# Optimization experiments

Measured on AMD Instinct MI355X. Metric: run time of the kernel, lower is better.

Reference implementation:

```python
import jax, jax.numpy as jnp
import numpy as np

BS, N = 64, 44            # batch, nodes per graph (fully connected)
H = 256                   # hidden_nf
N_LAYERS = 4              # equivariant blocks
INV_SUB = 2               # GCL sublayers per block
IN_H = 7                  # h feature dim incl. time channel (in_node_nf)
REP_NF = 512
NORM_FACTOR = 100.0       # normalization_factor, aggregation='sum'


def setup_inputs() -> dict:
    key = jax.random.key(0)
    ks = jax.random.split(key, 24)
    f32 = jnp.float32
    def rn(k, shape, s=0.02):
        return jax.random.normal(k, shape, f32) * s
    G = N_LAYERS * INV_SUB
    inp = {}
    inp['t'] = jax.random.uniform(ks[0], (BS, 1), f32)
    inp['xh'] = jax.random.normal(ks[1], (BS, N, 9), f32)
    inp['node_mask'] = jnp.ones((BS, N, 1), f32)
    # fully-connected edge mask with self-edges removed (standard EDM setup)
    inp['edge_mask'] = jnp.ones((BS, N, N, 1), f32) * (1.0 - jnp.eye(N, dtype=f32))[None, :, :, None]
    inp['rep'] = jax.random.normal(ks[2], (BS, REP_NF), f32)
    # parameters
    inp['W_embed'] = rn(ks[3], (IN_H, H)); inp['b_embed'] = jnp.zeros((H,), f32)
    inp['W_rep'] = rn(ks[4], (REP_NF, H)); inp['b_rep'] = jnp.zeros((H,), f32)
    # GCL stacks (edge_attr has 2 features: current + initial squared distance)
    inp['We1'] = rn(ks[5], (G, 2 * H + 2, H)); inp['be1'] = jnp.zeros((G, H), f32)
    inp['We2'] = rn(ks[6], (G, H, H));         inp['be2'] = jnp.zeros((G, H), f32)
    inp['Wn1'] = rn(ks[7], (G, 2 * H, H));     inp['bn1'] = jnp.zeros((G, H), f32)
    inp['Wn2'] = rn(ks[8], (G, H, H));         inp['bn2'] = jnp.zeros((G, H), f32)
    # coordinate-update MLP stacks (last layer bias-free, small init)
    inp['Wc1'] = rn(ks[9], (N_LAYERS, 2 * H + 2, H)); inp['bc1'] = jnp.zeros((N_LAYERS, H), f32)
    inp['Wc2'] = rn(ks[10], (N_LAYERS, H, H));        inp['bc2'] = jnp.zeros((N_LAYERS, H), f32)
    inp['Wc3'] = rn(ks[11], (N_LAYERS, H, 1), s=0.001)
    inp['W_out'] = rn(ks[12], (H, IN_H)); inp['b_out'] = jnp.zeros((IN_H,), f32)
    return inp


def _coord2diff(x):
    diff = x[:, :, None, :] - x[:, None, :, :]           # [bs,n,n,3]
    radial = jnp.sum(diff * diff, -1, keepdims=True)     # [bs,n,n,1] squared distance
    coord_diff = diff / jnp.sqrt(radial + 1e-8)          # norm_constant = 0
    return radial, coord_diff


def reference(t, xh, node_mask, edge_mask, rep,
              W_embed, b_embed, W_rep, b_rep,
              We1, be1, We2, be2, Wn1, bn1, Wn2, bn2,
              Wc1, bc1, Wc2, bc2, Wc3, W_out, b_out):
    silu = jax.nn.silu
    bs, n, _ = xh.shape
    xh = xh * node_mask
    x0 = xh[..., :3]
    h = xh[..., 3:]
    # condition_time: append per-graph time broadcast to nodes
    h = jnp.concatenate([h, jnp.broadcast_to(t[:, None, :], (bs, n, 1))], -1)
    # node embedding + per-graph rep conditioning (GeoRCG)
    h = h @ W_embed + b_embed + (rep @ W_rep + b_rep)[:, None, :]

    d0, _ = _coord2diff(x0)   # initial squared distances, reused as edge_attr base
    x = x0
    k = 0
    for l in range(N_LAYERS):
        d, cdiff = _coord2diff(x)
        ea = jnp.concatenate([d, d0], -1)                 # [bs,n,n,2]
        for _s in range(INV_SUB):
            hi = jnp.broadcast_to(h[:, :, None, :], (bs, n, n, H))
            hj = jnp.broadcast_to(h[:, None, :, :], (bs, n, n, H))
            e_in = jnp.concatenate([hi, hj, ea], -1)      # [bs,n,n,2H+2]
            m = silu(silu(e_in @ We1[k] + be1[k]) @ We2[k] + be2[k])
            m = m * edge_mask
            agg = jnp.sum(m, axis=2) / NORM_FACTOR        # scatter-sum over senders j
            h = h + (silu(jnp.concatenate([h, agg], -1) @ Wn1[k] + bn1[k]) @ Wn2[k] + bn2[k])
            h = h * node_mask
            k += 1
        # equivariant coordinate update
        hi = jnp.broadcast_to(h[:, :, None, :], (bs, n, n, H))
        hj = jnp.broadcast_to(h[:, None, :, :], (bs, n, n, H))
        e_in = jnp.concatenate([hi, hj, ea], -1)
        phi = silu(silu(e_in @ Wc1[l] + bc1[l]) @ Wc2[l] + bc2[l]) @ Wc3[l]  # [bs,n,n,1]
        trans = cdiff * phi * edge_mask
        x = (x + jnp.sum(trans, axis=2) / NORM_FACTOR) * node_mask

    h = (h @ W_out + b_out) * node_mask
    h_final = h[..., :-1]                                 # strip time channel
    vel = (x - x0) * node_mask
    # remove_mean_with_mask
    Nn = jnp.sum(node_mask, axis=1, keepdims=True)
    vel = (vel - jnp.sum(vel, axis=1, keepdims=True) / Nn) * node_mask
    return jnp.concatenate([vel, h_final], -1)            # [bs,n,9]
```

## Files before the change

kernel.cpp:

```cpp
#include <hip/hip_runtime.h>

typedef __bf16 bf16_t;
typedef __bf16 bf16x8 __attribute__((ext_vector_type(8)));
typedef float  f32x4  __attribute__((ext_vector_type(4)));

#define BSZ 64
#define NNODE 44
#define NODES (BSZ*NNODE)

__device__ __forceinline__ float  bf2f(bf16_t v){ return (float)v; }
__device__ __forceinline__ bf16_t f2bf(float v){ return (bf16_t)v; }
__device__ __forceinline__ float  silu_f(float v){ return v / (1.0f + __expf(-v)); }

__global__ void transpose_wb(const float* __restrict__ src, bf16_t* __restrict__ dst,
                             int R, int ldo) {
  __shared__ bf16_t tile[32][33];
  int g = blockIdx.z;
  src += (size_t)g * R * 256;
  dst += (size_t)g * 256 * ldo;
  int n0 = blockIdx.x * 32, r0 = blockIdx.y * 32;
  int tx = threadIdx.x, ty = threadIdx.y;
  for (int p = 0; p < 32; p += 8) {
    int r = r0 + ty + p;
    if (r < R) tile[ty + p][tx] = f2bf(src[(size_t)r * 256 + n0 + tx]);
  }
  __syncthreads();
  for (int p = 0; p < 32; p += 8) {
    int r = r0 + tx;
    if (r < R) dst[(size_t)(n0 + ty + p) * ldo + r] = tile[tx][ty + p];
  }
}

__global__ __launch_bounds__(256)
void repproj_kernel(const float* __restrict__ rep, const float* __restrict__ W_rep,
                    const float* __restrict__ b_rep, float* __restrict__ out) {
  int b = blockIdx.x, c = threadIdx.x;
  float acc = b_rep[c];
  const float* r = rep + (size_t)b * 512;
  for (int k = 0; k < 512; k++) acc += r[k] * W_rep[(size_t)k * 256 + c];
  out[(size_t)b * 256 + c] = acc;
}

__global__ __launch_bounds__(256)
void embed_kernel(const float* __restrict__ xh, const float* __restrict__ t,
                  const float* __restrict__ nmask,
                  const float* __restrict__ W_embed, const float* __restrict__ b_embed,
                  const float* __restrict__ repproj,
                  float* __restrict__ h_f32, bf16_t* __restrict__ cat1,
                  float* __restrict__ x0, float* __restrict__ x) {
  int m = blockIdx.x;
  int b = m / NNODE;
  int c = threadIdx.x;
  float nm = nmask[m];
  float acc = b_embed[c] + repproj[(size_t)b * 256 + c];
  for (int kk = 0; kk < 6; kk++)
    acc += xh[(size_t)m * 9 + 3 + kk] * nm * W_embed[(size_t)kk * 256 + c];
  acc += t[b] * W_embed[6 * 256 + c];
  h_f32[(size_t)m * 256 + c] = acc;
  cat1 [(size_t)m * 512 + c] = f2bf(acc);
  if (c < 3) {
    float xv = xh[(size_t)m * 9 + c] * nm;
    x0[(size_t)m * 3 + c] = xv;
    x [(size_t)m * 3 + c] = xv;
  }
}

template<int MODE>
__global__ __launch_bounds__(256)
void gemm_node(const bf16_t* __restrict__ A, int lda,
               const bf16_t* __restrict__ BT, int ldbt,
               const float* __restrict__ bias, size_t ob, int K,
               float* __restrict__ outPQ,
               bf16_t* __restrict__ outB,
               const float* __restrict__ hold,
               float* __restrict__ hnew,
               bf16_t* __restrict__ catb,
               const float* __restrict__ nmask) {
  int tid = threadIdx.x;
  int m0 = blockIdx.y * 64, n0 = blockIdx.x * 64;
  int kof = (MODE == 0) ? (int)blockIdx.z * 256 : 0;
  int w = tid >> 6, lane = tid & 63, q = lane >> 4, lr = lane & 15;
  int wm = w & 1, wn = w >> 1;
  f32x4 acc[2][2];
  for (int a = 0; a < 2; a++) for (int bb = 0; bb < 2; bb++)
    for (int rr = 0; rr < 4; rr++) acc[a][bb][rr] = 0.0f;
  const bf16_t* Arow0 = A  + (size_t)(m0 + wm * 32 + lr) * lda;
  const bf16_t* Brow0 = BT + (size_t)(n0 + wn * 32 + lr) * ldbt + kof;
  for (int k0 = 0; k0 < K; k0 += 32) {
    bf16x8 af[2], bfr[2];
    for (int mt = 0; mt < 2; mt++)
      af[mt]  = *(const bf16x8*)(Arow0 + (size_t)mt * 16 * lda + k0 + q * 8);
    for (int nt = 0; nt < 2; nt++)
      bfr[nt] = *(const bf16x8*)(Brow0 + (size_t)nt * 16 * ldbt + k0 + q * 8);
    for (int mt = 0; mt < 2; mt++)
      for (int nt = 0; nt < 2; nt++)
        acc[mt][nt] = __builtin_amdgcn_mfma_f32_16x16x32_bf16(af[mt], bfr[nt], acc[mt][nt], 0, 0, 0);
  }
  for (int mt = 0; mt < 2; mt++)
    for (int nt = 0; nt < 2; nt++) {
      int col = n0 + wn * 32 + nt * 16 + lr;
      for (int rr = 0; rr < 4; rr++) {
        int row = m0 + wm * 32 + mt * 16 + q * 4 + rr;
        float v = acc[mt][nt][rr];
        if constexpr (MODE == 0) {
          outPQ[(size_t)row * 512 + (size_t)blockIdx.z * 256 + col] = v;
        } else if constexpr (MODE == 1) {
          v = silu_f(v + bias[ob + col]);
          outB[(size_t)row * 256 + col] = f2bf(v);
        } else {
          v = v + bias[ob + col] + hold[(size_t)row * 256 + col];
          v *= nmask[row];
          hnew[(size_t)row * 256 + col] = v;
          catb[(size_t)row * 512 + col] = f2bf(v);
        }
      }
    }
}

template<int COORD>
__global__ __launch_bounds__(256)
void edge_kernel(const float* __restrict__ PQ,
                 const float* __restrict__ We1raw, size_t oW1,
                 const float* __restrict__ be1,   size_t ob1,
                 const bf16_t* __restrict__ W2T,  size_t oW2,
                 const float* __restrict__ b2,    size_t ob2,
                 const float* __restrict__ wc3,   size_t oc3,
                 const float* __restrict__ xcur,
                 const float* __restrict__ x0g,
                 const float* __restrict__ emask,
                 const float* __restrict__ nmask,
                 bf16_t* __restrict__ aggout,
                 float* __restrict__ xnext) {
  __shared__ __align__(16) bf16_t Ae[48][264];
  __shared__ float  xjL[48][3], x0jL[48][3];
  __shared__ float2 ddL[48];
  __shared__ float  emLDS[48];
  __shared__ float  phiLDS[4][48];
  int ni = blockIdx.x;
  int b = ni / NNODE;
  int i = ni % NNODE;
  size_t e0 = (size_t)ni * NNODE;
  int tid = threadIdx.x;
  if (tid < NNODE) {
    for (int c = 0; c < 3; c++) {
      xjL [tid][c] = xcur[(size_t)(b * NNODE + tid) * 3 + c];
      x0jL[tid][c] = x0g [(size_t)(b * NNODE + tid) * 3 + c];
    }
  }
  if (tid < 48) emLDS[tid] = (tid < NNODE) ? emask[e0 + tid] : 0.f;
  __syncthreads();
  if (tid < NNODE) {
    float dx = xjL[i][0] - xjL[tid][0];
    float dy = xjL[i][1] - xjL[tid][1];
    float dz = xjL[i][2] - xjL[tid][2];
    float dd = dx * dx + dy * dy + dz * dz;
    float ex = x0jL[i][0] - x0jL[tid][0];
    float ey = x0jL[i][1] - x0jL[tid][1];
    float ez = x0jL[i][2] - x0jL[tid][2];
    float dd0 = ex * ex + ey * ey + ez * ez;
    ddL[tid] = make_float2(dd, dd0);
  }
  __syncthreads();
  {
    int n = tid;
    float pi_b = PQ[(size_t)ni * 512 + n] + be1[ob1 + n];
    float w512 = We1raw[oW1 + 512 * 256 + n];
    float w513 = We1raw[oW1 + 513 * 256 + n];
    const float* qptr = PQ + (size_t)(b * NNODE) * 512 + 256 + n;
    #pragma unroll 4
    for (int j = 0; j < NNODE; j++) {
      float2 dd = ddL[j];
      float v = silu_f(pi_b + qptr[(size_t)j * 512] + dd.x * w512 + dd.y * w513);
      Ae[j][n] = f2bf(v);
    }
    for (int j = NNODE; j < 48; j++) Ae[j][n] = (bf16_t)0.f;
  }
  __syncthreads();
  int w = tid >> 6, lane = tid & 63, q = lane >> 4, lr = lane & 15;
  f32x4 acc[3][4];
  for (int mt = 0; mt < 3; mt++) for (int nt = 0; nt < 4; nt++)
    for (int rr = 0; rr < 4; rr++) acc[mt][nt][rr] = 0.0f;
  const bf16_t* Bbase = W2T + oW2 + (size_t)(w * 64 + lr) * 256;
  #pragma unroll
  for (int kk = 0; kk < 256; kk += 32) {
    bf16x8 af[3], bfr[4];
    for (int mt = 0; mt < 3; mt++)
      af[mt]  = *(const bf16x8*)(&Ae[mt * 16 + lr][kk + q * 8]);
    for (int nt = 0; nt < 4; nt++)
      bfr[nt] = *(const bf16x8*)(Bbase + (size_t)nt * 16 * 256 + kk + q * 8);
    for (int mt = 0; mt < 3; mt++)
      for (int nt = 0; nt < 4; nt++)
        acc[mt][nt] = __builtin_amdgcn_mfma_f32_16x16x32_bf16(af[mt], bfr[nt], acc[mt][nt], 0, 0, 0);
  }
  if constexpr (!COORD) {
    for (int nt = 0; nt < 4; nt++) {
      int col = w * 64 + nt * 16 + lr;
      float bcol = b2[ob2 + col];
      float s = 0.f;
      for (int mt = 0; mt < 3; mt++)
        for (int rr = 0; rr < 4; rr++) {
          int row = mt * 16 + q * 4 + rr;
          s += silu_f(acc[mt][nt][rr] + bcol) * emLDS[row];
        }
      s += __shfl_xor(s, 16, 64);
      s += __shfl_xor(s, 32, 64);
      if (q == 0) aggout[(size_t)ni * 512 + 256 + col] = f2bf(s * 0.01f);
    }
  } else {
    for (int mt = 0; mt < 3; mt++) {
      float rs[4] = {0.f, 0.f, 0.f, 0.f};
      for (int nt = 0; nt < 4; nt++) {
        int col = w * 64 + nt * 16 + lr;
        float bcol = b2[ob2 + col];
        float wc   = wc3[oc3 + col];
        for (int rr = 0; rr < 4; rr++)
          rs[rr] += silu_f(acc[mt][nt][rr] + bcol) * wc;
      }
      for (int off = 1; off <= 8; off <<= 1)
        for (int rr = 0; rr < 4; rr++) rs[rr] += __shfl_xor(rs[rr], off, 64);
      if (lr == 0)
        for (int rr = 0; rr < 4; rr++)
          phiLDS[w][mt * 16 + q * 4 + rr] = rs[rr];
    }
    __syncthreads();
    if (tid < 64) {
      int j = lane;
      float tx = 0.f, ty = 0.f, tz = 0.f;
      if (j < NNODE) {
        float ph = 0.f;
        for (int ww = 0; ww < 4; ww++) ph += phiLDS[ww][j];
        ph *= emLDS[j];
        float dx = xjL[i][0] - xjL[j][0];
        float dy = xjL[i][1] - xjL[j][1];
        float dz = xjL[i][2] - xjL[j][2];
        float dd = dx * dx + dy * dy + dz * dz;
        float rinv = 1.0f / sqrtf(dd + 1e-8f);
        tx = ph * dx * rinv;
        ty = ph * dy * rinv;
        tz = ph * dz * rinv;
      }
      for (int off = 1; off <= 32; off <<= 1) {
        tx += __shfl_xor(tx, off, 64);
        ty += __shfl_xor(ty, off, 64);
        tz += __shfl_xor(tz, off, 64);
      }
      if (lane == 0) {
        float nm = nmask[ni];
        xnext[(size_t)ni * 3 + 0] = (xjL[i][0] + tx * 0.01f) * nm;
        xnext[(size_t)ni * 3 + 1] = (xjL[i][1] + ty * 0.01f) * nm;
        xnext[(size_t)ni * 3 + 2] = (xjL[i][2] + tz * 0.01f) * nm;
      }
    }
  }
}

__global__ __launch_bounds__(256)
void out_kernel(const float* __restrict__ h, const float* __restrict__ x,
                const float* __restrict__ x0, const float* __restrict__ nmask,
                const float* __restrict__ W_out, const float* __restrict__ b_out,
                float* __restrict__ out) {
  __shared__ float vel[NNODE][3];
  __shared__ float sums[4];
  int b = blockIdx.x, tid = threadIdx.x;
  if (tid < NNODE * 3) {
    int n = tid / 3, c = tid % 3;
    int m = b * NNODE + n;
    vel[n][c] = (x[(size_t)m * 3 + c] - x0[(size_t)m * 3 + c]) * nmask[m];
  }
  __syncthreads();
  if (tid < 4) {
    float s = 0.f;
    if (tid < 3) { for (int n = 0; n < NNODE; n++) s += vel[n][tid]; }
    else         { for (int n = 0; n < NNODE; n++) s += nmask[b * NNODE + n]; }
    sums[tid] = s;
  }
  __syncthreads();
  if (tid < NNODE * 3) {
    int n = tid / 3, c = tid % 3;
    int m = b * NNODE + n;
    float v = (vel[n][c] - sums[c] / sums[3]) * nmask[m];
    out[(size_t)m * 9 + c] = v;
  }
  for (int idx = tid; idx < NNODE * 6; idx += 256) {
    int n = idx / 6, c = idx % 6;
    int m = b * NNODE + n;
    float accv = b_out[c];
    const float* hr = h + (size_t)m * 256;
    for (int k = 0; k < 256; k++) accv += hr[k] * W_out[(size_t)k * 7 + c];
    out[(size_t)m * 9 + 3 + c] = accv * nmask[m];
  }
}

extern "C" void kernel_launch(void* const* d_in, const int* in_sizes, int n_in,
                              void* d_out, int out_size, void* d_ws, size_t ws_size,
                              hipStream_t stream) {
  const float* t       = (const float*)d_in[0];
  const float* xh      = (const float*)d_in[1];
  const float* nmask   = (const float*)d_in[2];
  const float* emask   = (const float*)d_in[3];
  const float* rep     = (const float*)d_in[4];
  const float* W_embed = (const float*)d_in[5];
  const float* b_embed = (const float*)d_in[6];
  const float* W_rep   = (const float*)d_in[7];
  const float* b_rep   = (const float*)d_in[8];
  const float* We1     = (const float*)d_in[9];
  const float* be1     = (const float*)d_in[10];
  const float* We2     = (const float*)d_in[11];
  const float* be2     = (const float*)d_in[12];
  const float* Wn1     = (const float*)d_in[13];
  const float* bn1     = (const float*)d_in[14];
  const float* Wn2     = (const float*)d_in[15];
  const float* bn2     = (const float*)d_in[16];
  const float* Wc1     = (const float*)d_in[17];
  const float* bc1     = (const float*)d_in[18];
  const float* Wc2     = (const float*)d_in[19];
  const float* bc2     = (const float*)d_in[20];
  const float* Wc3     = (const float*)d_in[21];
  const float* W_out   = (const float*)d_in[22];
  const float* b_out   = (const float*)d_in[23];

  char* p = (char*)d_ws;
  auto alloc = [&](size_t bytes) { char* r = p; p += (bytes + 255) & ~(size_t)255; return r; };
  bf16_t* We1T  = (bf16_t*)alloc((size_t)8 * 256 * 520 * 2);
  bf16_t* Wc1T  = (bf16_t*)alloc((size_t)4 * 256 * 520 * 2);
  bf16_t* We2T  = (bf16_t*)alloc((size_t)8 * 256 * 256 * 2);
  bf16_t* Wc2T  = (bf16_t*)alloc((size_t)4 * 256 * 256 * 2);
  bf16_t* Wn1T  = (bf16_t*)alloc((size_t)8 * 256 * 512 * 2);
  bf16_t* Wn2T  = (bf16_t*)alloc((size_t)8 * 256 * 256 * 2);
  float*  h_f32 = (float*) alloc((size_t)NODES * 256 * 4);
  bf16_t* cat1  = (bf16_t*)alloc((size_t)NODES * 512 * 2);
  bf16_t* t1    = (bf16_t*)alloc((size_t)NODES * 256 * 2);
  float*  PQ    = (float*) alloc((size_t)NODES * 512 * 4);
  float*  x0buf = (float*) alloc((size_t)NODES * 3 * 4);
  float*  xA    = (float*) alloc((size_t)NODES * 3 * 4);
  float*  xB    = (float*) alloc((size_t)NODES * 3 * 4);
  float*  rproj = (float*) alloc((size_t)BSZ * 256 * 4);

  dim3 tb(32, 8);
  transpose_wb<<<dim3(8, 17, 8), tb, 0, stream>>>(We1, We1T, 514, 520);
  transpose_wb<<<dim3(8, 17, 4), tb, 0, stream>>>(Wc1, Wc1T, 514, 520);
  transpose_wb<<<dim3(8,  8, 8), tb, 0, stream>>>(We2, We2T, 256, 256);
  transpose_wb<<<dim3(8,  8, 4), tb, 0, stream>>>(Wc2, Wc2T, 256, 256);
  transpose_wb<<<dim3(8, 16, 8), tb, 0, stream>>>(Wn1, Wn1T, 512, 512);
  transpose_wb<<<dim3(8,  8, 8), tb, 0, stream>>>(Wn2, Wn2T, 256, 256);

  repproj_kernel<<<BSZ, 256, 0, stream>>>(rep, W_rep, b_rep, rproj);
  embed_kernel<<<NODES, 256, 0, stream>>>(xh, t, nmask, W_embed, b_embed, rproj,
                                          h_f32, cat1, x0buf, xA);

  float* xcur = xA;
  for (int l = 0; l < 4; l++) {
    float* xnext = (l & 1) ? xA : xB;
    for (int s = 0; s < 2; s++) {
      int k = 2 * l + s;
      size_t oWe1 = (size_t)k * 514 * 256, obe1 = (size_t)k * 256;
      size_t oWe2 = (size_t)k * 256 * 256, obe2 = (size_t)k * 256;
      size_t obn1 = (size_t)k * 256, obn2 = (size_t)k * 256;
      gemm_node<0><<<dim3(4, 44, 2), 256, 0, stream>>>(
          cat1, 512, We1T + (size_t)k * 256 * 520, 520, nullptr, 0, 256,
          PQ, nullptr, nullptr, nullptr, nullptr, nullptr);
      edge_kernel<0><<<NODES, 256, 0, stream>>>(
          PQ, We1, oWe1, be1, obe1, We2T, oWe2, be2, obe2, Wc3, 0,
          xcur, x0buf, emask, nmask, cat1, nullptr);
      gemm_node<1><<<dim3(4, 44, 1), 256, 0, stream>>>(
          cat1, 512, Wn1T + (size_t)k * 256 * 512, 512, bn1, obn1, 512,
          nullptr, t1, nullptr, nullptr, nullptr, nullptr);
      gemm_node<2><<<dim3(4, 44, 1), 256, 0, stream>>>(
          t1, 256, Wn2T + (size_t)k * 256 * 256, 256, bn2, obn2, 256,
          nullptr, nullptr, h_f32, h_f32, cat1, nmask);
    }
    size_t oWc1 = (size_t)l * 514 * 256, obc1 = (size_t)l * 256;
    size_t oWc2 = (size_t)l * 256 * 256, obc2 = (size_t)l * 256;
    size_t oc3  = (size_t)l * 256;
    gemm_node<0><<<dim3(4, 44, 2), 256, 0, stream>>>(
        cat1, 512, Wc1T + (size_t)l * 256 * 520, 520, nullptr, 0, 256,
        PQ, nullptr, nullptr, nullptr, nullptr, nullptr);
    edge_kernel<1><<<NODES, 256, 0, stream>>>(
        PQ, Wc1, oWc1, bc1, obc1, Wc2T, oWc2, bc2, obc2, Wc3, oc3,
        xcur, x0buf, emask, nmask, nullptr, xnext);
    xcur = xnext;
  }

  out_kernel<<<BSZ, 256, 0, stream>>>(h_f32, xcur, x0buf, nmask, W_out, b_out,
                                      (float*)d_out);
}
```

Baseline: 1.233 ms.

## Fuse node MLP GEMMs and process two receiver nodes per edge block

New measurement: 1.239 ms. About the same (+0.5%).

```diff
diff --git a/kernel.cpp b/kernel.cpp
--- a/kernel.cpp
+++ b/kernel.cpp
@@ -65,20 +65,13 @@
   }
 }
 
-template<int MODE>
 __global__ __launch_bounds__(256)
-void gemm_node(const bf16_t* __restrict__ A, int lda,
-               const bf16_t* __restrict__ BT, int ldbt,
-               const float* __restrict__ bias, size_t ob, int K,
-               float* __restrict__ outPQ,
-               bf16_t* __restrict__ outB,
-               const float* __restrict__ hold,
-               float* __restrict__ hnew,
-               bf16_t* __restrict__ catb,
-               const float* __restrict__ nmask) {
+void gemm_pq(const bf16_t* __restrict__ A, int lda,
+             const bf16_t* __restrict__ BT, int ldbt,
+             float* __restrict__ outPQ) {
   int tid = threadIdx.x;
   int m0 = blockIdx.y * 64, n0 = blockIdx.x * 64;
-  int kof = (MODE == 0) ? (int)blockIdx.z * 256 : 0;
+  int kof = (int)blockIdx.z * 256;
   int w = tid >> 6, lane = tid & 63, q = lane >> 4, lr = lane & 15;
   int wm = w & 1, wn = w >> 1;
   f32x4 acc[2][2];
@@ -86,7 +79,7 @@
     for (int rr = 0; rr < 4; rr++) acc[a][bb][rr] = 0.0f;
   const bf16_t* Arow0 = A  + (size_t)(m0 + wm * 32 + lr) * lda;
   const bf16_t* Brow0 = BT + (size_t)(n0 + wn * 32 + lr) * ldbt + kof;
-  for (int k0 = 0; k0 < K; k0 += 32) {
+  for (int k0 = 0; k0 < 256; k0 += 32) {
     bf16x8 af[2], bfr[2];
     for (int mt = 0; mt < 2; mt++)
       af[mt]  = *(const bf16x8*)(Arow0 + (size_t)mt * 16 * lda + k0 + q * 8);
@@ -101,27 +94,81 @@
       int col = n0 + wn * 32 + nt * 16 + lr;
       for (int rr = 0; rr < 4; rr++) {
         int row = m0 + wm * 32 + mt * 16 + q * 4 + rr;
-        float v = acc[mt][nt][rr];
-        if constexpr (MODE == 0) {
-          outPQ[(size_t)row * 512 + (size_t)blockIdx.z * 256 + col] = v;
-        } else if constexpr (MODE == 1) {
-          v = silu_f(v + bias[ob + col]);
-          outB[(size_t)row * 256 + col] = f2bf(v);
-        } else {
-          v = v + bias[ob + col] + hold[(size_t)row * 256 + col];
-          v *= nmask[row];
-          hnew[(size_t)row * 256 + col] = v;
-          catb[(size_t)row * 512 + col] = f2bf(v);
-        }
+        outPQ[(size_t)row * 512 + (size_t)blockIdx.z * 256 + col] = acc[mt][nt][rr];
+      }
+    }
+}
+
+__global__ __launch_bounds__(256)
+void node_mlp(const bf16_t* __restrict__ cat1,
+              const bf16_t* __restrict__ Wn1T,
+              const float* __restrict__ bn1, size_t ob1,
+              const bf16_t* __restrict__ Wn2T,
+              const float* __restrict__ bn2, size_t ob2,
+              const float* __restrict__ nmask,
+              float* __restrict__ h, bf16_t* __restrict__ catb) {
+  __shared__ __align__(16) bf16_t t1s[64][264];
+  int tid = threadIdx.x;
+  int m0 = blockIdx.x * 64;
+  int w = tid >> 6, lane = tid & 63, q = lane >> 4, lr = lane & 15;
+  f32x4 acc[4][4];
+  for (int mt = 0; mt < 4; mt++) for (int nt = 0; nt < 4; nt++)
+    for (int rr = 0; rr < 4; rr++) acc[mt][nt][rr] = 0.0f;
+  const bf16_t* Arow = cat1 + (size_t)(m0 + lr) * 512;
+  const bf16_t* Brow = Wn1T + (size_t)(w * 64 + lr) * 512;
+  for (int k0 = 0; k0 < 512; k0 += 32) {
+    bf16x8 af[4], bfr[4];
+    for (int mt = 0; mt < 4; mt++)
+      af[mt]  = *(const bf16x8*)(Arow + (size_t)mt * 16 * 512 + k0 + q * 8);
+    for (int nt = 0; nt < 4; nt++)
+      bfr[nt] = *(const bf16x8*)(Brow + (size_t)nt * 16 * 512 + k0 + q * 8);
+    for (int mt = 0; mt < 4; mt++)
+      for (int nt = 0; nt < 4; nt++)
+        acc[mt][nt] = __builtin_amdgcn_mfma_f32_16x16x32_bf16(af[mt], bfr[nt], acc[mt][nt], 0, 0, 0);
+  }
+  for (int mt = 0; mt < 4; mt++)
+    for (int nt = 0; nt < 4; nt++) {
+      int col = w * 64 + nt * 16 + lr;
+      float bc = bn1[ob1 + col];
+      for (int rr = 0; rr < 4; rr++) {
+        int row = mt * 16 + q * 4 + rr;
+        t1s[row][col] = f2bf(silu_f(acc[mt][nt][rr] + bc));
+      }
+    }
+  __syncthreads();
+  f32x4 acc2[4][4];
+  for (int mt = 0; mt < 4; mt++) for (int nt = 0; nt < 4; nt++)
+    for (int rr = 0; rr < 4; rr++) acc2[mt][nt][rr] = 0.0f;
+  const bf16_t* Brow2 = Wn2T + (size_t)(w * 64 + lr) * 256;
+  for (int k0 = 0; k0 < 256; k0 += 32) {
+    bf16x8 af[4], bfr[4];
+    for (int mt = 0; mt < 4; mt++)
+      af[mt]  = *(const bf16x8*)(&t1s[mt * 16 + lr][k0 + q * 8]);
+    for (int nt = 0; nt < 4; nt++)
+      bfr[nt] = *(const bf16x8*)(Brow2 + (size_t)nt * 16 * 256 + k0 + q * 8);
+    for (int mt = 0; mt < 4; mt++)
+      for (int nt = 0; nt < 4; nt++)
+        acc2[mt][nt] = __builtin_amdgcn_mfma_f32_16x16x32_bf16(af[mt], bfr[nt], acc2[mt][nt], 0, 0, 0);
+  }
+  for (int mt = 0; mt < 4; mt++)
+    for (int nt = 0; nt < 4; nt++) {
+      int col = w * 64 + nt * 16 + lr;
+      float bc = bn2[ob2 + col];
+      for (int rr = 0; rr < 4; rr++) {
+        int row = m0 + mt * 16 + q * 4 + rr;
+        float v = acc2[mt][nt][rr] + bc + h[(size_t)row * 256 + col];
+        v *= nmask[row];
+        h[(size_t)row * 256 + col] = v;
+        catb[(size_t)row * 512 + col] = f2bf(v);
       }
     }
 }
 
 template<int COORD>
-__global__ __launch_bounds__(256)
+__global__ __launch_bounds__(512, 4)
 void edge_kernel(const float* __restrict__ PQ,
+                 const float* __restrict__ be1,   size_t ob1,
                  const float* __restrict__ We1raw, size_t oW1,
-                 const float* __restrict__ be1,   size_t ob1,
                  const bf16_t* __restrict__ W2T,  size_t oW2,
                  const float* __restrict__ b2,    size_t ob2,
                  const float* __restrict__ wc3,   size_t oc3,
@@ -131,15 +178,14 @@
                  const float* __restrict__ nmask,
                  bf16_t* __restrict__ aggout,
                  float* __restrict__ xnext) {
-  __shared__ __align__(16) bf16_t Ae[48][264];
+  __shared__ __align__(16) bf16_t Ae[96][264];
   __shared__ float  xjL[48][3], x0jL[48][3];
-  __shared__ float2 ddL[48];
-  __shared__ float  emLDS[48];
-  __shared__ float  phiLDS[4][48];
-  int ni = blockIdx.x;
-  int b = ni / NNODE;
-  int i = ni % NNODE;
-  size_t e0 = (size_t)ni * NNODE;
+  __shared__ float2 ddL[2][48];
+  __shared__ float  emLDS[2][48];
+  __shared__ float  phiLDS[8][96];
+  int bp = blockIdx.x;
+  int b  = bp / 22;
+  int ip = (bp % 22) * 2;
   int tid = threadIdx.x;
   if (tid < NNODE) {
     for (int c = 0; c < 3; c++) {
@@ -147,70 +193,85 @@
       x0jL[tid][c] = x0g [(size_t)(b * NNODE + tid) * 3 + c];
     }
   }
-  if (tid < 48) emLDS[tid] = (tid < NNODE) ? emask[e0 + tid] : 0.f;
-  __syncthreads();
-  if (tid < NNODE) {
-    float dx = xjL[i][0] - xjL[tid][0];
-    float dy = xjL[i][1] - xjL[tid][1];
-    float dz = xjL[i][2] - xjL[tid][2];
-    float dd = dx * dx + dy * dy + dz * dz;
-    float ex = x0jL[i][0] - x0jL[tid][0];
-    float ey = x0jL[i][1] - x0jL[tid][1];
-    float ez = x0jL[i][2] - x0jL[tid][2];
-    float dd0 = ex * ex + ey * ey + ez * ez;
-    ddL[tid] = make_float2(dd, dd0);
+  if (tid < 96) {
+    int ii = tid / 48, j = tid % 48;
+    emLDS[ii][j] = (j < NNODE) ? emask[(size_t)(b * NNODE + ip + ii) * NNODE + j] : 0.f;
+  }
+  __syncthreads();
+  if (tid < 96) {
+    int ii = tid / 48, j = tid % 48;
+    int i = ip + ii;
+    float2 r = make_float2(0.f, 0.f);
+    if (j < NNODE) {
+      float dx = xjL[i][0] - xjL[j][0];
+      float dy = xjL[i][1] - xjL[j][1];
+      float dz = xjL[i][2] - xjL[j][2];
+      r.x = dx * dx + dy * dy + dz * dz;
+      float ex = x0jL[i][0] - x0jL[j][0];
+      float ey = x0jL[i][1] - x0jL[j][1];
+      float ez = x0jL[i][2] - x0jL[j][2];
+      r.y = ex * ex + ey * ey + ez * ez;
+    }
+    ddL[ii][j] = r;
   }
   __syncthreads();
   {
-    int n = tid;
+    int n = tid & 255, half = tid >> 8;
+    int ni = b * NNODE + ip + half;
     float pi_b = PQ[(size_t)ni * 512 + n] + be1[ob1 + n];
     float w512 = We1raw[oW1 + 512 * 256 + n];
     float w513 = We1raw[oW1 + 513 * 256 + n];
     const float* qptr = PQ + (size_t)(b * NNODE) * 512 + 256 + n;
-    #pragma unroll 4
+    bf16_t* arow = &Ae[half * 48][0];
+    #pragma unroll 8
     for (int j = 0; j < NNODE; j++) {
-      float2 dd = ddL[j];
-      float v = silu_f(pi_b + qptr[(size_t)j * 512] + dd.x * w512 + dd.y * w513);
-      Ae[j][n] = f2bf(v);
-    }
-    for (int j = NNODE; j < 48; j++) Ae[j][n] = (bf16_t)0.f;
+      float qv = qptr[(size_t)j * 512];
+      float2 dd = ddL[half][j];
+      arow[(size_t)j * 264 + n] = f2bf(silu_f(pi_b + qv + dd.x * w512 + dd.y * w513));
+    }
+    for (int j = NNODE; j < 48; j++) arow[(size_t)j * 264 + n] = (bf16_t)0.f;
   }
   __syncthreads();
   int w = tid >> 6, lane = tid & 63, q = lane >> 4, lr = lane & 15;
-  f32x4 acc[3][4];
-  for (int mt = 0; mt < 3; mt++) for (int nt = 0; nt < 4; nt++)
+  f32x4 acc[6][2];
+  for (int mt = 0; mt < 6; mt++) for (int nt = 0; nt < 2; nt++)
     for (int rr = 0; rr < 4; rr++) acc[mt][nt][rr] = 0.0f;
-  const bf16_t* Bbase = W2T + oW2 + (size_t)(w * 64 + lr) * 256;
+  const bf16_t* Bbase = W2T + oW2 + (size_t)(w * 32 + lr) * 256;
   #pragma unroll
   for (int kk = 0; kk < 256; kk += 32) {
-    bf16x8 af[3], bfr[4];
-    for (int mt = 0; mt < 3; mt++)
+    bf16x8 af[6], bfr[2];
+    for (int mt = 0; mt < 6; mt++)
       af[mt]  = *(const bf16x8*)(&Ae[mt * 16 + lr][kk + q * 8]);
-    for (int nt = 0; nt < 4; nt++)
+    for (int nt = 0; nt < 2; nt++)
       bfr[nt] = *(const bf16x8*)(Bbase + (size_t)nt * 16 * 256 + kk + q * 8);
-    for (int mt = 0; mt < 3; mt++)
-      for (int nt = 0; nt < 4; nt++)
+    for (int mt = 0; mt < 6; mt++)
+      for (int nt = 0; nt < 2; nt++)
         acc[mt][nt] = __builtin_amdgcn_mfma_f32_16x16x32_bf16(af[mt], bfr[nt], acc[mt][nt], 0, 0, 0);
   }
   if constexpr (!COORD) {
-    for (int nt = 0; nt < 4; nt++) {
-      int col = w * 64 + nt * 16 + lr;
+    for (int nt = 0; nt < 2; nt++) {
+      int col = w * 32 + nt * 16 + lr;
       float bcol = b2[ob2 + col];
-      float s = 0.f;
+      float s0 = 0.f, s1 = 0.f;
       for (int mt = 0; mt < 3; mt++)
         for (int rr = 0; rr < 4; rr++) {
           int row = mt * 16 + q * 4 + rr;
-          s += silu_f(acc[mt][nt][rr] + bcol) * emLDS[row];
+          s0 += silu_f(acc[mt][nt][rr] + bcol) * emLDS[0][row];
+          s1 += silu_f(acc[mt + 3][nt][rr] + bcol) * emLDS[1][row];
         }
-      s += __shfl_xor(s, 16, 64);
-      s += __shfl_xor(s, 32, 64);
-      if (q == 0) aggout[(size_t)ni * 512 + 256 + col] = f2bf(s * 0.01f);
+      s0 += __shfl_xor(s0, 16, 64);  s0 += __shfl_xor(s0, 32, 64);
+      s1 += __shfl_xor(s1, 16, 64);  s1 += __shfl_xor(s1, 32, 64);
+      if (q == 0) {
+        size_t ni0 = (size_t)(b * NNODE + ip);
+        aggout[ni0 * 512 + 256 + col]       = f2bf(s0 * 0.01f);
+        aggout[(ni0 + 1) * 512 + 256 + col] = f2bf(s1 * 0.01f);
+      }
     }
   } else {
-    for (int mt = 0; mt < 3; mt++) {
+    for (int mt = 0; mt < 6; mt++) {
       float rs[4] = {0.f, 0.f, 0.f, 0.f};
-      for (int nt = 0; nt < 4; nt++) {
-        int col = w * 64 + nt * 16 + lr;
+      for (int nt = 0; nt < 2; nt++) {
+        int col = w * 32 + nt * 16 + lr;
         float bcol = b2[ob2 + col];
         float wc   = wc3[oc3 + col];
         for (int rr = 0; rr < 4; rr++)
@@ -223,13 +284,15 @@
           phiLDS[w][mt * 16 + q * 4 + rr] = rs[rr];
     }
     __syncthreads();
-    if (tid < 64) {
+    if (tid < 128) {
+      int ii = tid >> 6;
       int j = lane;
+      int i = ip + ii;
       float tx = 0.f, ty = 0.f, tz = 0.f;
       if (j < NNODE) {
         float ph = 0.f;
-        for (int ww = 0; ww < 4; ww++) ph += phiLDS[ww][j];
-        ph *= emLDS[j];
+        for (int ww = 0; ww < 8; ww++) ph += phiLDS[ww][ii * 48 + j];
+        ph *= emLDS[ii][j];
         float dx = xjL[i][0] - xjL[j][0];
         float dy = xjL[i][1] - xjL[j][1];
         float dz = xjL[i][2] - xjL[j][2];
@@ -245,10 +308,11 @@
         tz += __shfl_xor(tz, off, 64);
       }
       if (lane == 0) {
+        size_t ni = (size_t)(b * NNODE + i);
         float nm = nmask[ni];
-        xnext[(size_t)ni * 3 + 0] = (xjL[i][0] + tx * 0.01f) * nm;
-        xnext[(size_t)ni * 3 + 1] = (xjL[i][1] + ty * 0.01f) * nm;
-        xnext[(size_t)ni * 3 + 2] = (xjL[i][2] + tz * 0.01f) * nm;
+        xnext[ni * 3 + 0] = (xjL[i][0] + tx * 0.01f) * nm;
+        xnext[ni * 3 + 1] = (xjL[i][1] + ty * 0.01f) * nm;
+        xnext[ni * 3 + 2] = (xjL[i][2] + tz * 0.01f) * nm;
       }
     }
   }
@@ -329,7 +393,6 @@
   bf16_t* Wn2T  = (bf16_t*)alloc((size_t)8 * 256 * 256 * 2);
   float*  h_f32 = (float*) alloc((size_t)NODES * 256 * 4);
   bf16_t* cat1  = (bf16_t*)alloc((size_t)NODES * 512 * 2);
-  bf16_t* t1    = (bf16_t*)alloc((size_t)NODES * 256 * 2);
   float*  PQ    = (float*) alloc((size_t)NODES * 512 * 4);
   float*  x0buf = (float*) alloc((size_t)NODES * 3 * 4);
   float*  xA    = (float*) alloc((size_t)NODES * 3 * 4);
@@ -356,27 +419,22 @@
       size_t oWe1 = (size_t)k * 514 * 256, obe1 = (size_t)k * 256;
       size_t oWe2 = (size_t)k * 256 * 256, obe2 = (size_t)k * 256;
       size_t obn1 = (size_t)k * 256, obn2 = (size_t)k * 256;
-      gemm_node<0><<<dim3(4, 44, 2), 256, 0, stream>>>(
-          cat1, 512, We1T + (size_t)k * 256 * 520, 520, nullptr, 0, 256,
-          PQ, nullptr, nullptr, nullptr, nullptr, nullptr);
-      edge_kernel<0><<<NODES, 256, 0, stream>>>(
-          PQ, We1, oWe1, be1, obe1, We2T, oWe2, be2, obe2, Wc3, 0,
+      gemm_pq<<<dim3(4, 44, 2), 256, 0, stream>>>(
+          cat1, 512, We1T + (size_t)k * 256 * 520, 520, PQ);
+      edge_kernel<0><<<NODES / 2, 512, 0, stream>>>(
+          PQ, be1, obe1, We1, oWe1, We2T, oWe2, be2, obe2, Wc3, 0,
           xcur, x0buf, emask, nmask, cat1, nullptr);
-      gemm_node<1><<<dim3(4, 44, 1), 256, 0, stream>>>(
-          cat1, 512, Wn1T + (size_t)k * 256 * 512, 512, bn1, obn1, 512,
-          nullptr, t1, nullptr, nullptr, nullptr, nullptr);
-      gemm_node<2><<<dim3(4, 44, 1), 256, 0, stream>>>(
-          t1, 256, Wn2T + (size_t)k * 256 * 256, 256, bn2, obn2, 256,
-          nullptr, nullptr, h_f32, h_f32, cat1, nmask);
+      node_mlp<<<NODES / 64, 256, 0, stream>>>(
+          cat1, Wn1T + (size_t)k * 256 * 512, bn1, obn1,
+          Wn2T + (size_t)k * 256 * 256, bn2, obn2, nmask, h_f32, cat1);
     }
     size_t oWc1 = (size_t)l * 514 * 256, obc1 = (size_t)l * 256;
     size_t oWc2 = (size_t)l * 256 * 256, obc2 = (size_t)l * 256;
     size_t oc3  = (size_t)l * 256;
-    gemm_node<0><<<dim3(4, 44, 2), 256, 0, stream>>>(
-        cat1, 512, Wc1T + (size_t)l * 256 * 520, 520, nullptr, 0, 256,
-        PQ, nullptr, nullptr, nullptr, nullptr, nullptr);
-    edge_kernel<1><<<NODES, 256, 0, stream>>>(
-        PQ, Wc1, oWc1, bc1, obc1, Wc2T, oWc2, bc2, obc2, Wc3, oc3,
+    gemm_pq<<<dim3(4, 44, 2), 256, 0, stream>>>(
+        cat1, 512, Wc1T + (size_t)l * 256 * 520, 520, PQ);
+    edge_kernel<1><<<NODES / 2, 512, 0, stream>>>(
+        PQ, bc1, obc1, Wc1, oWc1, Wc2T, oWc2, bc2, obc2, Wc3, oc3,
         xcur, x0buf, emask, nmask, nullptr, xnext);
     xcur = xnext;
   }
```
